# Kernel tuning notes

Measured on AMD Instinct MI355X. Metric: run time of the kernel, lower is better.

## Reference

```python
import jax, jax.numpy as jnp
import numpy as np

# dims: B=1, T=2048 (prefill), dim=3072, Hq=32, Hkv=8, D=128, S=max_seq_len=4096

def _rotate_interleave(x):
    # (-x1, x0, -x3, x2, ...) pairwise rotation on last dim
    x = x.reshape(x.shape[:-1] + (-1, 2))
    x = jnp.stack((-x[..., 1], x[..., 0]), axis=-1)
    return x.reshape(x.shape[:-2] + (-1,))


def setup_inputs() -> dict:
    key = jax.random.key(0)
    ks = jax.random.split(key, 8)
    B, T, DIM, HQ, HKV, HD, S = 1, 2048, 3072, 32, 8, 128, 4096
    x = jax.random.normal(ks[0], (B, T, DIM), jnp.float32)
    wq = jax.random.normal(ks[1], (HQ * HD, DIM), jnp.float32) * 0.02
    wk = jax.random.normal(ks[2], (HKV * HD, DIM), jnp.float32) * 0.02
    wv = jax.random.normal(ks[3], (HKV * HD, DIM), jnp.float32) * 0.02
    wo = jax.random.normal(ks[4], (DIM, HQ * HD), jnp.float32) * 0.02
    freqs_cos = jax.random.uniform(ks[5], (T, HD), jnp.float32)
    freqs_sin = jax.random.uniform(ks[6], (T, HD), jnp.float32)
    input_pos = jnp.zeros((1,), jnp.int32)
    k_cache = jnp.zeros((1, S, HKV, HD), jnp.float32)
    v_cache = jnp.zeros((1, S, HKV, HD), jnp.float32)
    return {"x": x, "wq": wq, "wk": wk, "wv": wv, "wo": wo,
            "freqs_cos": freqs_cos, "freqs_sin": freqs_sin,
            "k_cache": k_cache, "v_cache": v_cache, "input_pos": input_pos}


def reference(x, wq, wk, wv, wo, freqs_cos, freqs_sin, k_cache, v_cache, input_pos):
    B, T, _ = x.shape
    HQ, HKV, HD = 32, 8, 128
    q = (x @ wq.T).reshape(B, T, HQ, HD)
    k = (x @ wk.T).reshape(B, T, HKV, HD)
    v = (x @ wv.T).reshape(B, T, HKV, HD)
    # interleaved RoPE (computed in fp32 as in apply_rotary_emb)
    fc = freqs_cos[None, :, None, :]
    fs = freqs_sin[None, :, None, :]
    q = q * fc + _rotate_interleave(q) * fs
    k = k * fc + _rotate_interleave(k) * fs
    # KV-cache update at start_pos (torch.ops.llama.update_cache)
    sp = input_pos[0]
    k_all = jax.lax.dynamic_update_slice(k_cache, k, (0, sp, 0, 0))  # [1,S,HKV,HD]
    v_all = jax.lax.dynamic_update_slice(v_cache, v, (0, sp, 0, 0))
    S = k_all.shape[1]
    # GQA: expand kv heads to match q heads (head h -> kv head h // rep)
    rep = HQ // HKV
    kr = jnp.repeat(k_all, rep, axis=2)  # [1,S,HQ,HD]
    vr = jnp.repeat(v_all, rep, axis=2)
    scale = 1.0 / np.sqrt(HD).astype(np.float32)
    scores = jnp.einsum('bthd,bshd->bhts', q, kr) * scale  # [B,HQ,T,S]
    # causal mask relative to start_pos (custom_sdpa is_causal=True path)
    qpos = sp + jnp.arange(T)
    kpos = jnp.arange(S)
    mask = kpos[None, :] <= qpos[:, None]                   # [T,S]
    scores = jnp.where(mask[None, None], scores, jnp.float32(-1e30))
    attn = jax.nn.softmax(scores, axis=-1)
    y = jnp.einsum('bhts,bshd->bthd', attn, vr).reshape(B, T, HQ * HD)
    return y @ wo.T
```

## Files before the change

### kernel.cpp

```cpp
#include <hip/hip_runtime.h>
#include <hip/hip_bf16.h>
#include <stdint.h>

typedef float f32x4 __attribute__((ext_vector_type(4)));
typedef short s16x8 __attribute__((ext_vector_type(8)));
typedef short s16x4 __attribute__((ext_vector_type(4)));
typedef unsigned short u16x2 __attribute__((ext_vector_type(2)));
typedef unsigned short u16x4 __attribute__((ext_vector_type(4)));

#define AS1 __attribute__((address_space(1)))
#define AS3 __attribute__((address_space(3)))

static constexpr int T_    = 2048;
static constexpr int DIM_  = 3072;
static constexpr int HQ_   = 32;
static constexpr int HKV_  = 8;
static constexpr int HD_   = 128;
static constexpr int S_    = 4096;
static constexpr int NQKV_ = HQ_ * HD_ + 2 * HKV_ * HD_;

__device__ __forceinline__ unsigned short f2b(float f) {
  return __builtin_bit_cast(unsigned short, __float2bfloat16(f));
}
__device__ __forceinline__ float b2f(unsigned short u) {
  return __bfloat162float(__builtin_bit_cast(__hip_bfloat16, u));
}
__device__ __forceinline__ float exp2a(float x) {
  float r; asm("v_exp_f32 %0, %1" : "=v"(r) : "v"(x)); return r;
}

__device__ __forceinline__ void gld_lds16(const void* g, void* l) {
  __builtin_amdgcn_global_load_lds((AS1 unsigned int*)(uintptr_t)g,
                                   (AS3 unsigned int*)l, 16, 0, 0);
}

#define FENCE() asm volatile("" ::: "memory")
#define BAR()   do { FENCE(); __builtin_amdgcn_s_barrier(); FENCE(); } while (0)
#define WAIT_VM(n)   asm volatile("s_waitcnt vmcnt(" #n ")" ::: "memory")
#define WAIT_LGKM(n) asm volatile("s_waitcnt lgkmcnt(" #n ")" ::: "memory")
#define SCHEDB()     __builtin_amdgcn_sched_barrier(0)

__global__ __launch_bounds__(256)
void k_cvt(const float* __restrict__ src, unsigned short* __restrict__ dst, int n4) {
  int i = blockIdx.x * 256 + threadIdx.x;
  if (i >= n4) return;
  float4 v = reinterpret_cast<const float4*>(src)[i];
  u16x4 o;
  o.x = f2b(v.x); o.y = f2b(v.y); o.z = f2b(v.z); o.w = f2b(v.w);
  reinterpret_cast<u16x4*>(dst)[i] = o;
}

template<bool OUT_BF16>
__global__ __launch_bounds__(512, 2)
void k_gemm256(const unsigned short* __restrict__ A,
               const unsigned short* __restrict__ B,
               void* __restrict__ Cout, int N, int K, int KT,
               int nbn, int xcdq, int k0step, int partStride) {
  __shared__ unsigned short lds_u[2][32768];
  char* ldsBase = (char*)&lds_u[0][0];

  const int bid = blockIdx.x;
  const int swz = (bid & 7) * xcdq + (bid >> 3);
  const int bm  = swz / nbn, bn = swz % nbn;
  const int tid = threadIdx.x, lane = tid & 63, wid = tid >> 6;
  const int wm  = wid >> 2, wn = wid & 3;
  const int r16 = lane & 15, q4 = lane >> 4;
  const int k0  = blockIdx.y * k0step;

  const unsigned short* Ag = A + (size_t)(bm * 256) * K + k0;
  const unsigned short* Bg = B + (size_t)(bn * 256) * K + k0;

  const int srow = tid >> 3;
  const int scol = ((tid & 7) ^ (srow & 7)) * 8;

  f32x4 acc[8][4] = {};
  s16x8 afA[4][2], afB[4][2], bfA[2][2], bfB[2][2];

  auto stageA = [&](int c, int r, int t) {
    gld_lds16(Ag + (size_t)(r * 64 + srow) * K + t * 64 + scol,
              ldsBase + c * 65536 + r * 8192 + tid * 16);
  };
  auto stageB = [&](int c, int r, int t) {
    gld_lds16(Bg + (size_t)(r * 64 + srow) * K + t * 64 + scol,
              ldsBase + c * 65536 + 32768 + r * 8192 + tid * 16);
  };
  auto stagePair = [&](int c, int pair, int t) {
    switch (pair) {
      case 0: stageB(c, 0, t); stageB(c, 1, t); break;
      case 1: stageB(c, 2, t); stageB(c, 3, t); break;
      case 2: stageA(c, 0, t); stageA(c, 2, t); break;
      case 3: stageA(c, 1, t); stageA(c, 3, t); break;
    }
  };
  auto readAF = [&](s16x8 (&dst)[4][2], char* base, int rowoff) {
    #pragma unroll
    for (int i = 0; i < 4; ++i) {
      const int arow = wm * 128 + rowoff + i * 16 + r16;
      #pragma unroll
      for (int kk = 0; kk < 2; ++kk)
        dst[i][kk] = *(const s16x8*)(base + arow * 128 +
                                     (((kk * 4 + q4) ^ (arow & 7)) << 4));
    }
  };
  auto readBF = [&](s16x8 (&dst)[2][2], char* base, int rowoff) {
    #pragma unroll
    for (int j = 0; j < 2; ++j) {
      const int brow = wn * 64 + rowoff + j * 16 + r16;
      #pragma unroll
      for (int kk = 0; kk < 2; ++kk)
        dst[j][kk] = *(const s16x8*)(base + 32768 + brow * 128 +
                                     (((kk * 4 + q4) ^ (brow & 7)) << 4));
    }
  };

#define MFMA16(AF, BF, IO, JO)                                                 \
  __builtin_amdgcn_s_setprio(1);                                               \
  _Pragma("unroll")                                                            \
  for (int i_ = 0; i_ < 4; ++i_) {                                             \
    _Pragma("unroll")                                                          \
    for (int j_ = 0; j_ < 2; ++j_) {                                           \
      _Pragma("unroll")                                                        \
      for (int kk_ = 0; kk_ < 2; ++kk_)                                        \
        acc[(IO) + i_][(JO) + j_] = __builtin_amdgcn_mfma_f32_16x16x32_bf16(   \
            AF[i_][kk_], BF[j_][kk_], acc[(IO) + i_][(JO) + j_], 0, 0, 0);     \
    }                                                                          \
  }                                                                            \
  __builtin_amdgcn_s_setprio(0);

  stagePair(0, 0, 0); stagePair(0, 1, 0); stagePair(0, 2, 0); stagePair(0, 3, 0);
  stagePair(1, 0, 1); stagePair(1, 1, 1);
  WAIT_VM(6);
  BAR();
  readAF(afA, ldsBase, 0);
  readBF(bfA, ldsBase, 0);

  for (int t = 0; t < KT - 2; ++t) {
    const int c = t & 1;
    char* baseC = ldsBase + c * 65536;
    char* baseN = ldsBase + (c ^ 1) * 65536;
    readBF(bfB, baseC, 32);
    stagePair(c ^ 1, 2, t + 1);
    WAIT_VM(6); BAR();
    WAIT_LGKM(4); SCHEDB();
    MFMA16(afA, bfA, 0, 0);
    BAR();
    readAF(afB, baseC, 64);
    stagePair(c ^ 1, 3, t + 1);
    BAR();
    WAIT_LGKM(8); SCHEDB();
    MFMA16(afA, bfB, 0, 2);
    BAR();
    stagePair(c, 0, t + 2);
    WAIT_VM(4); BAR();
    WAIT_LGKM(0); SCHEDB();
    MFMA16(afB, bfA, 4, 0);
    BAR();
    readAF(afA, baseN, 0);
    readBF(bfA, baseN, 0);
    stagePair(c, 1, t + 2);
    WAIT_VM(8); BAR();
    WAIT_LGKM(12); SCHEDB();
    MFMA16(afB, bfB, 4, 2);
    BAR();
  }
  {
    const int t = KT - 2;
    const int c = t & 1;
    char* baseC = ldsBase + c * 65536;
    char* baseN = ldsBase + (c ^ 1) * 65536;
    readBF(bfB, baseC, 32);
    stagePair(c ^ 1, 2, t + 1);
    WAIT_VM(6); BAR();
    WAIT_LGKM(4); SCHEDB();
    MFMA16(afA, bfA, 0, 0);
    BAR();
    readAF(afB, baseC, 64);
    stagePair(c ^ 1, 3, t + 1);
    BAR();
    WAIT_LGKM(8); SCHEDB();
    MFMA16(afA, bfB, 0, 2);
    BAR();
    WAIT_VM(2); BAR();
    WAIT_LGKM(0); SCHEDB();
    MFMA16(afB, bfA, 4, 0);
    BAR();
    readAF(afA, baseN, 0);
    readBF(bfA, baseN, 0);
    WAIT_VM(4); BAR();
    WAIT_LGKM(12); SCHEDB();
    MFMA16(afB, bfB, 4, 2);
    BAR();
  }
  {
    const int t = KT - 1;
    char* baseC = ldsBase + (t & 1) * 65536;
    readBF(bfB, baseC, 32);
    WAIT_VM(0); BAR();
    WAIT_LGKM(4); SCHEDB();
    MFMA16(afA, bfA, 0, 0);
    BAR();
    readAF(afB, baseC, 64);
    BAR();
    WAIT_LGKM(8); SCHEDB();
    MFMA16(afA, bfB, 0, 2);
    BAR();
    WAIT_LGKM(0); SCHEDB();
    MFMA16(afB, bfA, 4, 0);
    MFMA16(afB, bfB, 4, 2);
  }
#undef MFMA16

  #pragma unroll
  for (int fi = 0; fi < 8; ++fi) {
    const int row = bm * 256 + wm * 128 + fi * 16 + q4 * 4;
    #pragma unroll
    for (int fj = 0; fj < 4; ++fj) {
      const int col = bn * 256 + wn * 64 + fj * 16 + r16;
      if constexpr (OUT_BF16) {
        unsigned short* C = (unsigned short*)Cout;
        #pragma unroll
        for (int rr = 0; rr < 4; ++rr)
          C[(size_t)(row + rr) * N + col] = f2b(acc[fi][fj][rr]);
      } else {
        float* C = (float*)Cout + (size_t)blockIdx.y * partStride;
        #pragma unroll
        for (int rr = 0; rr < 4; ++rr)
          C[(size_t)(row + rr) * N + col] = acc[fi][fj][rr];
      }
    }
  }
}

__global__ __launch_bounds__(256)
void k_add(const f32x4* __restrict__ a, const f32x4* __restrict__ b,
           f32x4* __restrict__ o, int n4) {
  int i = blockIdx.x * 256 + threadIdx.x;
  const int stride = gridDim.x * 256;
  for (; i < n4; i += stride) o[i] = a[i] + b[i];
}

__global__ __launch_bounds__(256)
void k_rope_q(const unsigned short* __restrict__ qkv,
              const float* __restrict__ fc, const float* __restrict__ fs,
              unsigned short* __restrict__ Qr) {
  int idx = blockIdx.x * 256 + threadIdx.x;
  int t   = idx >> 11;
  int rem = idx & 2047;
  int h   = rem >> 6;
  int d0  = (rem & 63) << 1;
  size_t qoff = (size_t)t * NQKV_ + h * HD_ + d0;
  u16x2 xv = *reinterpret_cast<const u16x2*>(&qkv[qoff]);
  float x0 = b2f(xv.x), x1 = b2f(xv.y);
  float c0 = fc[t * HD_ + d0], c1 = fc[t * HD_ + d0 + 1];
  float s0 = fs[t * HD_ + d0], s1 = fs[t * HD_ + d0 + 1];
  u16x2 o;
  o.x = f2b(x0 * c0 - x1 * s0);
  o.y = f2b(x1 * c1 + x0 * s1);
  *reinterpret_cast<u16x2*>(&Qr[((size_t)h * T_ + t) * HD_ + d0]) = o;
}

__global__ __launch_bounds__(256)
void k_rope_k(const unsigned short* __restrict__ qkv,
              const float* __restrict__ fc, const float* __restrict__ fs,
              unsigned short* __restrict__ Kall, const int* __restrict__ ipos) {
  int idx = blockIdx.x * 256 + threadIdx.x;
  int t   = idx >> 9;
  int rem = idx & 511;
  int hk  = rem >> 6;
  int d0  = (rem & 63) << 1;
  int sp  = ipos[0];
  size_t qoff = (size_t)t * NQKV_ + HQ_ * HD_ + hk * HD_ + d0;
  u16x2 xv = *reinterpret_cast<const u16x2*>(&qkv[qoff]);
  float x0 = b2f(xv.x), x1 = b2f(xv.y);
  float c0 = fc[t * HD_ + d0], c1 = fc[t * HD_ + d0 + 1];
  float s0 = fs[t * HD_ + d0], s1 = fs[t * HD_ + d0 + 1];
  unsigned short o0 = f2b(x0 * c0 - x1 * s0);
  unsigned short o1 = f2b(x1 * c1 + x0 * s1);
  size_t ooff = ((size_t)hk * S_ + sp + t) * HD_ + d0;
  Kall[ooff] = o0; Kall[ooff + 1] = o1;
}

__global__ __launch_bounds__(256)
void k_prefix(const float* __restrict__ kc, const float* __restrict__ vc,
              unsigned short* __restrict__ Kall, unsigned short* __restrict__ VT,
              const int* __restrict__ ipos) {
  int sp = ipos[0];
  int total = sp * HKV_ * HD_;
  for (int idx = blockIdx.x * 256 + threadIdx.x; idx < total;
       idx += gridDim.x * 256) {
    int s   = idx >> 10;
    int rem = idx & 1023;
    int hk  = rem >> 7;
    int d   = rem & 127;
    Kall[((size_t)hk * S_ + s) * HD_ + d] = f2b(kc[((size_t)s * HKV_ + hk) * HD_ + d]);
    VT[((size_t)hk * HD_ + d) * S_ + s]   = f2b(vc[((size_t)s * HKV_ + hk) * HD_ + d]);
  }
}

__global__ __launch_bounds__(256)
void k_vt(const unsigned short* __restrict__ qkv,
          unsigned short* __restrict__ VT, const int* __restrict__ ipos) {
  int hk = blockIdx.x >> 5;
  int tt = blockIdx.x & 31;
  int sp = ipos[0];
  __shared__ unsigned short lds[64][136];
  int tid = threadIdx.x;
  #pragma unroll
  for (int p = 0; p < 4; ++p) {
    int e   = p * 256 + tid;
    int tr  = e >> 4;
    int col = (e & 15) << 3;
    *reinterpret_cast<s16x8*>(&lds[tr][col]) =
        *reinterpret_cast<const s16x8*>(&qkv[(size_t)(tt * 64 + tr) * NQKV_ + (HQ_ + HKV_) * HD_ + hk * HD_ + col]);
  }
  __syncthreads();
  #pragma unroll
  for (int p = 0; p < 32; ++p) {
    int e = p * 256 + tid;
    int d = e >> 6;
    int t = e & 63;
    VT[((size_t)hk * HD_ + d) * S_ + sp + tt * 64 + t] = lds[t][d];
  }
}

__global__ __launch_bounds__(256, 2)
void k_attn(const unsigned short* __restrict__ Qr,
            const unsigned short* __restrict__ Kall,
            const unsigned short* __restrict__ VT,
            unsigned short* __restrict__ Y,
            const int* __restrict__ ipos) {
  constexpr int QB = 64, KB = 64;
  __shared__ char lds[65536];
  const int bid  = blockIdx.x;
  const int hk   = bid & 7;
  const int j2   = bid >> 3;
  const int h    = hk * 4 + (j2 & 3);
  const int qt   = 31 - (j2 >> 2);
  const int tid  = threadIdx.x, lane = tid & 63, wave = tid >> 6;
  const int r16  = lane & 15, q4 = lane >> 4;
  const int vx   = r16 & 7;
  const float NEG_INF = -__builtin_inff();
  const float MINIT   = -1.0e30f;

  const int sp = ipos[0];
  const int qbase = qt * QB + wave * 16;
  const unsigned short* Kbase = Kall + (size_t)hk * S_ * HD_;
  const unsigned short* Vbase = VT + (size_t)hk * HD_ * S_;

  s16x8 qf[4];
  const unsigned short* qp = Qr + ((size_t)h * T_ + qbase + r16) * HD_;
  #pragma unroll
  for (int ki = 0; ki < 4; ++ki)
    qf[ki] = *reinterpret_cast<const s16x8*>(qp + ki * 32 + q4 * 8);
  SCHEDB(); WAIT_VM(0); SCHEDB();

  auto stage = [&](int c, int jt) {
    #pragma unroll
    for (int p = 0; p < 4; ++p) {
      int e  = p * 256 + tid;
      int kr = e >> 4;
      int ks = (e & 15) ^ (kr & 7);
      gld_lds16(Kbase + (size_t)(jt * KB + kr) * HD_ + ks * 8,
                lds + c * 16384 + e * 16);
    }
    #pragma unroll
    for (int p = 0; p < 4; ++p) {
      int e  = p * 256 + tid;
      int vd = e >> 3;
      int vs = (e & 7) ^ (vd & 7);
      gld_lds16(Vbase + (size_t)vd * S_ + jt * KB + vs * 8,
                lds + 32768 + c * 16384 + e * 16);
    }
  };

  f32x4 o[8] = {};
  float m = MINIT, l = 0.f;
  const int qpos = sp + qbase + r16;
  const int qpos_wave_max = sp + qbase + 15;
  int jmax = (sp + qt * QB + QB - 1) >> 6;
  if (jmax > S_ / KB - 1) jmax = S_ / KB - 1;
  const float scale2 = 0.12751744416312068f;

  stage(0, 0);

  for (int j = 0; j <= jmax; ++j) {
    const int c = j & 1;
    if (j < jmax) { stage(c ^ 1, j + 1); WAIT_VM(8); }
    else         { WAIT_VM(0); }
    BAR();

    const bool active = (j * KB <= qpos_wave_max);
    if (active) {
      const char* kb = lds + c * 16384;
      const char* vb = lds + 32768 + c * 16384;
      f32x4 sfr[4];
      #pragma unroll
      for (int fn = 0; fn < 4; ++fn) {
        sfr[fn] = f32x4{0.f, 0.f, 0.f, 0.f};
        #pragma unroll
        for (int ki = 0; ki < 4; ++ki) {
          s16x8 kf = *(const s16x8*)(kb + (fn * 16 + r16) * 256 +
                                     (((ki * 4 + q4) ^ vx) << 4));
          sfr[fn] = __builtin_amdgcn_mfma_f32_16x16x32_bf16(kf, qf[ki], sfr[fn], 0, 0, 0);
        }
      }
      float p[16];
      const bool needMask = (j * KB + KB - 1) > (sp + qbase);
      if (needMask) {
        const int kbp = j * KB + q4 * 4;
        #pragma unroll
        for (int fn = 0; fn < 4; ++fn)
          #pragma unroll
          for (int r = 0; r < 4; ++r)
            p[fn * 4 + r] = (kbp + fn * 16 + r <= qpos) ? sfr[fn][r] * scale2 : NEG_INF;
      } else {
        #pragma unroll
        for (int fn = 0; fn < 4; ++fn)
          #pragma unroll
          for (int r = 0; r < 4; ++r)
            p[fn * 4 + r] = sfr[fn][r] * scale2;
      }
      float pmax = p[0];
      #pragma unroll
      for (int i = 1; i < 16; ++i) pmax = fmaxf(pmax, p[i]);
      pmax = fmaxf(pmax, __shfl_xor(pmax, 16));
      pmax = fmaxf(pmax, __shfl_xor(pmax, 32));
      if (!__all(pmax <= m + 8.0f)) {
        float mn = fmaxf(m, pmax);
        float alpha = exp2a(m - mn);
        m = mn; l *= alpha;
        #pragma unroll
        for (int r = 0; r < 4; ++r) {
          float aq = __shfl(alpha, q4 * 4 + r);
          #pragma unroll
          for (int db = 0; db < 8; ++db) o[db][r] *= aq;
        }
      }
      float rs = 0.f;
      #pragma unroll
      for (int i = 0; i < 16; ++i) { p[i] = exp2a(p[i] - m); rs += p[i]; }
      rs += __shfl_xor(rs, 16); rs += __shfl_xor(rs, 32);
      l += rs;
      s16x8 pf[2];
      #pragma unroll
      for (int w = 0; w < 2; ++w)
        #pragma unroll
        for (int i = 0; i < 8; ++i)
          pf[w][i] = (short)f2b(p[w * 8 + i]);
      const int voff = (q4 & 1) * 8;
      const int sbase = q4 >> 1;
      #pragma unroll
      for (int w = 0; w < 2; ++w) {
        #pragma unroll
        for (int db = 0; db < 8; ++db) {
          const char* vr = vb + (db * 16 + r16) * 128 + voff;
          s16x4 va = *(const s16x4*)(vr + (((w * 4 + sbase) ^ vx) << 4));
          s16x4 vb2 = *(const s16x4*)(vr + (((w * 4 + 2 + sbase) ^ vx) << 4));
          s16x8 vf = __builtin_shufflevector(va, vb2, 0, 1, 2, 3, 4, 5, 6, 7);
          o[db] = __builtin_amdgcn_mfma_f32_16x16x32_bf16(pf[w], vf, o[db], 0, 0, 0);
        }
      }
    }
    BAR();
  }

  float rcpl = 1.0f / l;
  float rlq[4];
  #pragma unroll
  for (int r = 0; r < 4; ++r) rlq[r] = __shfl(rcpl, q4 * 4 + r);
  #pragma unroll
  for (int db = 0; db < 8; ++db)
    #pragma unroll
    for (int r = 0; r < 4; ++r) {
      int t = qt * QB + wave * 16 + q4 * 4 + r;
      int d = db * 16 + r16;
      Y[(size_t)t * (HQ_ * HD_) + h * HD_ + d] = f2b(o[db][r] * rlq[r]);
    }
}

extern "C" void kernel_launch(void* const* d_in, const int* in_sizes, int n_in,
                              void* d_out, int out_size, void* d_ws, size_t ws_size,
                              hipStream_t stream) {
  const float* x  = (const float*)d_in[0];
  const float* wq = (const float*)d_in[1];
  const float* wk = (const float*)d_in[2];
  const float* wv = (const float*)d_in[3];
  const float* wo = (const float*)d_in[4];
  const float* fc = (const float*)d_in[5];
  const float* fs = (const float*)d_in[6];
  const float* kc = (const float*)d_in[7];
  const float* vc = (const float*)d_in[8];
  const int* ipos = (const int*)d_in[9];

  char* ws = (char*)d_ws;
  unsigned short* xb   = (unsigned short*)(ws);
  unsigned short* wqkv = (unsigned short*)(ws + 12582912);
  unsigned short* qkv  = (unsigned short*)(ws + 50331648);
  unsigned short* Qr   = (unsigned short*)(ws + 75497472);
  unsigned short* Kall = (unsigned short*)(ws + 92274688);
  unsigned short* VT   = (unsigned short*)(ws + 100663296);
  unsigned short* wo_b = (unsigned short*)(ws);
  unsigned short* y    = qkv;

  float* part0 = (float*)(ws + 12582912);
  float* part1 = (float*)(ws + 75497472);
  const int partStrideElems = (75497472 - 12582912) / 4;

  k_cvt<<<6144, 256, 0, stream>>>(x, xb, 6291456 / 4);
  k_cvt<<<12288, 256, 0, stream>>>(wq, wqkv, 12582912 / 4);
  k_cvt<<<3072, 256, 0, stream>>>(wk, wqkv + 12582912, 3145728 / 4);
  k_cvt<<<3072, 256, 0, stream>>>(wv, wqkv + 15728640, 3145728 / 4);

  k_gemm256<true><<<192, 512, 0, stream>>>(xb, wqkv, qkv, NQKV_, DIM_, 48, 24, 24, 0, 0);

  k_cvt<<<12288, 256, 0, stream>>>(wo, wo_b, 12582912 / 4);

  k_rope_q<<<16384, 256, 0, stream>>>(qkv, fc, fs, Qr);
  k_rope_k<<<4096, 256, 0, stream>>>(qkv, fc, fs, Kall, ipos);
  k_prefix<<<2048, 256, 0, stream>>>(kc, vc, Kall, VT, ipos);
  k_vt<<<256, 256, 0, stream>>>(qkv, VT, ipos);

  k_attn<<<1024, 256, 0, stream>>>(Qr, Kall, VT, y, ipos);

  k_gemm256<false><<<dim3(96, 2), 512, 0, stream>>>(y, wo_b, part0, DIM_, HQ_ * HD_,
                                                    32, 12, 12, 2048, partStrideElems);
  k_add<<<1024, 256, 0, stream>>>((const f32x4*)part0, (const f32x4*)part1,
                                  (f32x4*)d_out, 6291456 / 4);
}
```

Before: 287.3 us.

## Replace 256x256 GEMM with 128x192 tiles, drop split-K and fuse weight converts

After: 273.9 us. -4.7%, faster.

```diff
diff --git a/kernel.cpp b/kernel.cpp
--- a/kernel.cpp
+++ b/kernel.cpp
@@ -50,193 +50,139 @@
   reinterpret_cast<u16x4*>(dst)[i] = o;
 }
 
+__global__ __launch_bounds__(256)
+void k_cvtW(const float* __restrict__ wq, const float* __restrict__ wk,
+            const float* __restrict__ wv, unsigned short* __restrict__ dst) {
+  int idx = blockIdx.x * 256 + threadIdx.x;
+  if (idx >= 4718592) return;
+  const float* src; int s;
+  if (idx < 3145728)      { src = wq; s = idx; }
+  else if (idx < 3932160) { src = wk; s = idx - 3145728; }
+  else                    { src = wv; s = idx - 3932160; }
+  float4 v = reinterpret_cast<const float4*>(src)[s];
+  u16x4 o;
+  o.x = f2b(v.x); o.y = f2b(v.y); o.z = f2b(v.z); o.w = f2b(v.w);
+  reinterpret_cast<u16x4*>(dst)[idx] = o;
+}
+
 template<bool OUT_BF16>
-__global__ __launch_bounds__(512, 2)
-void k_gemm256(const unsigned short* __restrict__ A,
+__global__ __launch_bounds__(512, 4)
+void k_gemm192(const unsigned short* __restrict__ A,
                const unsigned short* __restrict__ B,
                void* __restrict__ Cout, int N, int K, int KT,
-               int nbn, int xcdq, int k0step, int partStride) {
-  __shared__ unsigned short lds_u[2][32768];
-  char* ldsBase = (char*)&lds_u[0][0];
-
+               int nbn, int xcdq) {
+  __shared__ char lds[81920];
   const int bid = blockIdx.x;
   const int swz = (bid & 7) * xcdq + (bid >> 3);
   const int bm  = swz / nbn, bn = swz % nbn;
   const int tid = threadIdx.x, lane = tid & 63, wid = tid >> 6;
   const int wm  = wid >> 2, wn = wid & 3;
   const int r16 = lane & 15, q4 = lane >> 4;
-  const int k0  = blockIdx.y * k0step;
-
-  const unsigned short* Ag = A + (size_t)(bm * 256) * K + k0;
-  const unsigned short* Bg = B + (size_t)(bn * 256) * K + k0;
+
+  const unsigned short* Ag = A + (size_t)(bm * 128) * K;
+  const unsigned short* Bg = B + (size_t)(bn * 192) * K;
 
   const int srow = tid >> 3;
   const int scol = ((tid & 7) ^ (srow & 7)) * 8;
 
-  f32x4 acc[8][4] = {};
-  s16x8 afA[4][2], afB[4][2], bfA[2][2], bfB[2][2];
+  f32x4 acc[4][3] = {};
+  s16x8 af[4][2];
 
   auto stageA = [&](int c, int r, int t) {
     gld_lds16(Ag + (size_t)(r * 64 + srow) * K + t * 64 + scol,
-              ldsBase + c * 65536 + r * 8192 + tid * 16);
+              lds + c * 40960 + r * 8192 + tid * 16);
   };
   auto stageB = [&](int c, int r, int t) {
     gld_lds16(Bg + (size_t)(r * 64 + srow) * K + t * 64 + scol,
-              ldsBase + c * 65536 + 32768 + r * 8192 + tid * 16);
+              lds + c * 40960 + 16384 + r * 8192 + tid * 16);
   };
-  auto stagePair = [&](int c, int pair, int t) {
-    switch (pair) {
-      case 0: stageB(c, 0, t); stageB(c, 1, t); break;
-      case 1: stageB(c, 2, t); stageB(c, 3, t); break;
-      case 2: stageA(c, 0, t); stageA(c, 2, t); break;
-      case 3: stageA(c, 1, t); stageA(c, 3, t); break;
+  auto readA = [&](int c) {
+    #pragma unroll
+    for (int i = 0; i < 4; ++i) {
+      const int arow = wm * 64 + i * 16 + r16;
+      #pragma unroll
+      for (int kk = 0; kk < 2; ++kk)
+        af[i][kk] = *(const s16x8*)(lds + c * 40960 + arow * 128 +
+                                    (((kk * 4 + q4) ^ (arow & 7)) << 4));
     }
   };
-  auto readAF = [&](s16x8 (&dst)[4][2], char* base, int rowoff) {
-    #pragma unroll
-    for (int i = 0; i < 4; ++i) {
-      const int arow = wm * 128 + rowoff + i * 16 + r16;
-      #pragma unroll
-      for (int kk = 0; kk < 2; ++kk)
-        dst[i][kk] = *(const s16x8*)(base + arow * 128 +
-                                     (((kk * 4 + q4) ^ (arow & 7)) << 4));
-    }
+  auto readB = [&](s16x8 (&dst)[2], int c, int j) {
+    const int brow = wn * 48 + j * 16 + r16;
+    #pragma unroll
+    for (int kk = 0; kk < 2; ++kk)
+      dst[kk] = *(const s16x8*)(lds + c * 40960 + 16384 + brow * 128 +
+                                (((kk * 4 + q4) ^ (brow & 7)) << 4));
   };
-  auto readBF = [&](s16x8 (&dst)[2][2], char* base, int rowoff) {
-    #pragma unroll
-    for (int j = 0; j < 2; ++j) {
-      const int brow = wn * 64 + rowoff + j * 16 + r16;
-      #pragma unroll
-      for (int kk = 0; kk < 2; ++kk)
-        dst[j][kk] = *(const s16x8*)(base + 32768 + brow * 128 +
-                                     (((kk * 4 + q4) ^ (brow & 7)) << 4));
-    }
-  };
-
-#define MFMA16(AF, BF, IO, JO)                                                 \
+
+#define MFMA8(BF, J)                                                           \
   __builtin_amdgcn_s_setprio(1);                                               \
   _Pragma("unroll")                                                            \
   for (int i_ = 0; i_ < 4; ++i_) {                                             \
     _Pragma("unroll")                                                          \
-    for (int j_ = 0; j_ < 2; ++j_) {                                           \
-      _Pragma("unroll")                                                        \
-      for (int kk_ = 0; kk_ < 2; ++kk_)                                        \
-        acc[(IO) + i_][(JO) + j_] = __builtin_amdgcn_mfma_f32_16x16x32_bf16(   \
-            AF[i_][kk_], BF[j_][kk_], acc[(IO) + i_][(JO) + j_], 0, 0, 0);     \
-    }                                                                          \
+    for (int kk_ = 0; kk_ < 2; ++kk_)                                          \
+      acc[i_][J] = __builtin_amdgcn_mfma_f32_16x16x32_bf16(                    \
+          af[i_][kk_], BF[kk_], acc[i_][J], 0, 0, 0);                          \
   }                                                                            \
   __builtin_amdgcn_s_setprio(0);
 
-  stagePair(0, 0, 0); stagePair(0, 1, 0); stagePair(0, 2, 0); stagePair(0, 3, 0);
-  stagePair(1, 0, 1); stagePair(1, 1, 1);
-  WAIT_VM(6);
+  stageA(0, 0, 0); stageA(0, 1, 0);
+  stageB(0, 0, 0); stageB(0, 1, 0); stageB(0, 2, 0);
+  WAIT_VM(0);
   BAR();
-  readAF(afA, ldsBase, 0);
-  readBF(bfA, ldsBase, 0);
-
-  for (int t = 0; t < KT - 2; ++t) {
+
+  for (int t = 0; t < KT; ++t) {
     const int c = t & 1;
-    char* baseC = ldsBase + c * 65536;
-    char* baseN = ldsBase + (c ^ 1) * 65536;
-    readBF(bfB, baseC, 32);
-    stagePair(c ^ 1, 2, t + 1);
-    WAIT_VM(6); BAR();
-    WAIT_LGKM(4); SCHEDB();
-    MFMA16(afA, bfA, 0, 0);
-    BAR();
-    readAF(afB, baseC, 64);
-    stagePair(c ^ 1, 3, t + 1);
-    BAR();
-    WAIT_LGKM(8); SCHEDB();
-    MFMA16(afA, bfB, 0, 2);
-    BAR();
-    stagePair(c, 0, t + 2);
-    WAIT_VM(4); BAR();
-    WAIT_LGKM(0); SCHEDB();
-    MFMA16(afB, bfA, 4, 0);
-    BAR();
-    readAF(afA, baseN, 0);
-    readBF(bfA, baseN, 0);
-    stagePair(c, 1, t + 2);
-    WAIT_VM(8); BAR();
-    WAIT_LGKM(12); SCHEDB();
-    MFMA16(afB, bfB, 4, 2);
-    BAR();
-  }
-  {
-    const int t = KT - 2;
-    const int c = t & 1;
-    char* baseC = ldsBase + c * 65536;
-    char* baseN = ldsBase + (c ^ 1) * 65536;
-    readBF(bfB, baseC, 32);
-    stagePair(c ^ 1, 2, t + 1);
-    WAIT_VM(6); BAR();
-    WAIT_LGKM(4); SCHEDB();
-    MFMA16(afA, bfA, 0, 0);
-    BAR();
-    readAF(afB, baseC, 64);
-    stagePair(c ^ 1, 3, t + 1);
-    BAR();
-    WAIT_LGKM(8); SCHEDB();
-    MFMA16(afA, bfB, 0, 2);
-    BAR();
-    WAIT_VM(2); BAR();
-    WAIT_LGKM(0); SCHEDB();
-    MFMA16(afB, bfA, 4, 0);
-    BAR();
-    readAF(afA, baseN, 0);
-    readBF(bfA, baseN, 0);
-    WAIT_VM(4); BAR();
-    WAIT_LGKM(12); SCHEDB();
-    MFMA16(afB, bfB, 4, 2);
-    BAR();
-  }
-  {
-    const int t = KT - 1;
-    char* baseC = ldsBase + (t & 1) * 65536;
-    readBF(bfB, baseC, 32);
-    WAIT_VM(0); BAR();
-    WAIT_LGKM(4); SCHEDB();
-    MFMA16(afA, bfA, 0, 0);
-    BAR();
-    readAF(afB, baseC, 64);
-    BAR();
-    WAIT_LGKM(8); SCHEDB();
-    MFMA16(afA, bfB, 0, 2);
-    BAR();
-    WAIT_LGKM(0); SCHEDB();
-    MFMA16(afB, bfA, 4, 0);
-    MFMA16(afB, bfB, 4, 2);
-  }
-#undef MFMA16
-
-  #pragma unroll
-  for (int fi = 0; fi < 8; ++fi) {
-    const int row = bm * 256 + wm * 128 + fi * 16 + q4 * 4;
-    #pragma unroll
-    for (int fj = 0; fj < 4; ++fj) {
-      const int col = bn * 256 + wn * 64 + fj * 16 + r16;
+    const bool hn = (t + 1 < KT);
+    {
+      s16x8 bfc[2];
+      readA(c); readB(bfc, c, 0);
+      if (hn) { stageA(c ^ 1, 0, t + 1); stageA(c ^ 1, 1, t + 1); }
+      BAR();
+      WAIT_LGKM(0); SCHEDB();
+      MFMA8(bfc, 0);
+      BAR();
+    }
+    {
+      s16x8 bfc[2];
+      readB(bfc, c, 1);
+      if (hn) { stageB(c ^ 1, 0, t + 1); stageB(c ^ 1, 1, t + 1); }
+      BAR();
+      WAIT_LGKM(0); SCHEDB();
+      MFMA8(bfc, 1);
+      BAR();
+    }
+    {
+      s16x8 bfc[2];
+      readB(bfc, c, 2);
+      if (hn) stageB(c ^ 1, 2, t + 1);
+      BAR();
+      WAIT_LGKM(0); SCHEDB();
+      MFMA8(bfc, 2);
+      if (hn) { WAIT_VM(0); }
+      BAR();
+    }
+  }
+#undef MFMA8
+
+  #pragma unroll
+  for (int i = 0; i < 4; ++i) {
+    const int row = bm * 128 + wm * 64 + i * 16 + q4 * 4;
+    #pragma unroll
+    for (int j = 0; j < 3; ++j) {
+      const int col = bn * 192 + wn * 48 + j * 16 + r16;
       if constexpr (OUT_BF16) {
         unsigned short* C = (unsigned short*)Cout;
         #pragma unroll
         for (int rr = 0; rr < 4; ++rr)
-          C[(size_t)(row + rr) * N + col] = f2b(acc[fi][fj][rr]);
+          C[(size_t)(row + rr) * N + col] = f2b(acc[i][j][rr]);
       } else {
-        float* C = (float*)Cout + (size_t)blockIdx.y * partStride;
+        float* C = (float*)Cout;
         #pragma unroll
         for (int rr = 0; rr < 4; ++rr)
-          C[(size_t)(row + rr) * N + col] = acc[fi][fj][rr];
+          C[(size_t)(row + rr) * N + col] = acc[i][j][rr];
       }
     }
   }
-}
-
-__global__ __launch_bounds__(256)
-void k_add(const f32x4* __restrict__ a, const f32x4* __restrict__ b,
-           f32x4* __restrict__ o, int n4) {
-  int i = blockIdx.x * 256 + threadIdx.x;
-  const int stride = gridDim.x * 256;
-  for (; i < n4; i += stride) o[i] = a[i] + b[i];
 }
 
 __global__ __launch_bounds__(256)
@@ -502,16 +448,10 @@
   unsigned short* wo_b = (unsigned short*)(ws);
   unsigned short* y    = qkv;
 
-  float* part0 = (float*)(ws + 12582912);
-  float* part1 = (float*)(ws + 75497472);
-  const int partStrideElems = (75497472 - 12582912) / 4;
-
   k_cvt<<<6144, 256, 0, stream>>>(x, xb, 6291456 / 4);
-  k_cvt<<<12288, 256, 0, stream>>>(wq, wqkv, 12582912 / 4);
-  k_cvt<<<3072, 256, 0, stream>>>(wk, wqkv + 12582912, 3145728 / 4);
-  k_cvt<<<3072, 256, 0, stream>>>(wv, wqkv + 15728640, 3145728 / 4);
-
-  k_gemm256<true><<<192, 512, 0, stream>>>(xb, wqkv, qkv, NQKV_, DIM_, 48, 24, 24, 0, 0);
+  k_cvtW<<<18432, 256, 0, stream>>>(wq, wk, wv, wqkv);
+
+  k_gemm192<true><<<512, 512, 0, stream>>>(xb, wqkv, qkv, NQKV_, DIM_, 48, 32, 64);
 
   k_cvt<<<12288, 256, 0, stream>>>(wo, wo_b, 12582912 / 4);
 
@@ -522,8 +462,5 @@
 
   k_attn<<<1024, 256, 0, stream>>>(Qr, Kall, VT, y, ipos);
 
-  k_gemm256<false><<<dim3(96, 2), 512, 0, stream>>>(y, wo_b, part0, DIM_, HQ_ * HD_,
-                                                    32, 12, 12, 2048, partStrideElems);
-  k_add<<<1024, 256, 0, stream>>>((const f32x4*)part0, (const f32x4*)part1,
-                                  (f32x4*)d_out, 6291456 / 4);
-}
+  k_gemm192<false><<<256, 512, 0, stream>>>(y, wo_b, d_out, DIM_, HQ_ * HD_, 64, 16, 32);
+}
```
